# Optimization experiments

Hardware: AMD Instinct MI355X
Metric: run time of the kernel (lower is better)

Reference implementation:

```python
import jax, jax.numpy as jnp
import numpy as np

NUM_HEADS = 4
EPS = 1e-5

def _proj(x, W, b):
    # 1x1x1 Conv3d == channel-wise linear: x [B,C,H,W,D], W [Cout,Cin], b [Cout]
    return jnp.einsum('oc,bchwd->bohwd', W, x) + b[None, :, None, None, None]

def setup_inputs() -> dict:
    key = jax.random.key(0)
    ks = jax.random.split(key, 12)
    B, C, H, W, D = 2, 128, 16, 16, 16
    s = 1.0 / np.sqrt(C)
    inp = {
        'query_features': jax.random.normal(ks[0], (B, C, H, W, D), jnp.float32),
        'key_value_features': jax.random.normal(ks[1], (B, C, H, W, D), jnp.float32),
        'Wq': jax.random.normal(ks[2], (C, C), jnp.float32) * s,
        'bq': jax.random.normal(ks[3], (C,), jnp.float32) * 0.01,
        'Wk': jax.random.normal(ks[4], (C, C), jnp.float32) * s,
        'bk': jax.random.normal(ks[5], (C,), jnp.float32) * 0.01,
        'Wv': jax.random.normal(ks[6], (C, C), jnp.float32) * s,
        'bv': jax.random.normal(ks[7], (C,), jnp.float32) * 0.01,
        'Wo': jax.random.normal(ks[8], (C, C), jnp.float32) * s,
        'bo': jax.random.normal(ks[9], (C,), jnp.float32) * 0.01,
    }
    return inp

def reference(query_features, key_value_features, Wq, bq, Wk, bk, Wv, bv, Wo, bo):
    B, C, H, W, D = query_features.shape
    hd = C // NUM_HEADS  # head_dim
    N = H * W * D
    Q = _proj(query_features, Wq, bq).reshape(B, NUM_HEADS, hd, N)
    K = _proj(key_value_features, Wk, bk).reshape(B, NUM_HEADS, hd, N)
    V = _proj(key_value_features, Wv, bv).reshape(B, NUM_HEADS, hd, N)
    scale = hd ** -0.5
    attn = jnp.einsum('bhdn,bhdm->bhnm', Q, K) * scale  # [B,h,N,N]
    attn = jax.nn.softmax(attn, axis=-1)
    out = jnp.einsum('bhnm,bhdm->bhdn', attn, V).reshape(B, C, H, W, D)
    out = _proj(out, Wo, bo)
    res = query_features + out
    # InstanceNorm3d (affine=False): normalize over spatial dims per (B,C)
    mu = jnp.mean(res, axis=(2, 3, 4), keepdims=True)
    var = jnp.var(res, axis=(2, 3, 4), keepdims=True)
    return (res - mu) * jax.lax.rsqrt(var + EPS)
```

## Files before the change

### kernel.cpp

```cpp
#include <hip/hip_runtime.h>
#include <hip/hip_bf16.h>

typedef unsigned short u16;
typedef unsigned int u32;
typedef __bf16 bf16_t;
typedef bf16_t bf16x8 __attribute__((ext_vector_type(8)));
typedef float f32x4 __attribute__((ext_vector_type(4)));

#define NTOT 4096
#define CCH 128
#define QSCL 0.25503486703f

__device__ __forceinline__ float bf2f(u16 x) {
    return __uint_as_float(((u32)x) << 16);
}
__device__ __forceinline__ u32 pkbf(float a, float b) {
    __hip_bfloat162 h = __float22bfloat162_rn(make_float2(a, b));
    u32 r; __builtin_memcpy(&r, &h, 4); return r;
}
__device__ __forceinline__ u16 f2bf(float a) {
    return (u16)(pkbf(a, a) & 0xffffu);
}

__global__ __launch_bounds__(256, 4) void proj_kernel(
    const float* __restrict__ xq, const float* __restrict__ xkv,
    const float* __restrict__ Wq, const float* __restrict__ bq,
    const float* __restrict__ Wk, const float* __restrict__ bk_,
    const float* __restrict__ Wv, const float* __restrict__ bv_,
    u16* __restrict__ Qt, u16* __restrict__ Kt, u16* __restrict__ Vn)
{
    const int nt = blockIdx.x, p = blockIdx.y, b = blockIdx.z;
    const float* X    = (p == 0) ? xq : xkv;
    const float* Wf   = (p == 0) ? Wq : (p == 1) ? Wk : Wv;
    const float* bias = (p == 0) ? bq : (p == 1) ? bk_ : bv_;
    const float s = (p == 0) ? QSCL : 1.0f;
    const int n0 = nt * 64;
    const int tid = threadIdx.x;

    __shared__ u16 Xt[64 * 128];
    __shared__ u16 Wl[128 * 136];

    #pragma unroll
    for (int k = 0; k < 4; ++k) {
        int n = tid & 63;
        int c = (tid >> 6) + k * 4;
        float f[8];
        #pragma unroll
        for (int j = 0; j < 8; ++j)
            f[j] = X[((size_t)(b * CCH) + 8 * c + j) * NTOT + n0 + n];
        uint4 vv = {pkbf(f[0], f[1]), pkbf(f[2], f[3]), pkbf(f[4], f[5]), pkbf(f[6], f[7])};
        *(uint4*)(Xt + n * 128 + ((c ^ (n & 7)) * 8)) = vv;
    }
    #pragma unroll
    for (int k = 0; k < 8; ++k) {
        int id = tid + k * 256;
        int row = id >> 4;
        int off = (id & 15) * 8;
        const float* wsrc = Wf + row * 128 + off;
        float4 wa = *(const float4*)(wsrc);
        float4 wc = *(const float4*)(wsrc + 4);
        uint4 vv = {pkbf(wa.x * s, wa.y * s), pkbf(wa.z * s, wa.w * s),
                    pkbf(wc.x * s, wc.y * s), pkbf(wc.z * s, wc.w * s)};
        *(uint4*)(Wl + row * 136 + off) = vv;
    }
    __syncthreads();

    const int wave = tid >> 6, lane = tid & 63;
    const int quad = lane >> 4, l16 = lane & 15;
    f32x4 acc[8];
    #pragma unroll
    for (int cf = 0; cf < 8; ++cf) acc[cf] = (f32x4){0.f, 0.f, 0.f, 0.f};

    #pragma unroll
    for (int kk = 0; kk < 4; ++kk) {
        bf16x8 bx = *(const bf16x8*)(Xt + (wave * 16 + l16) * 128 +
                                     (((kk * 4 + quad) ^ (l16 & 7)) * 8));
        #pragma unroll
        for (int cf = 0; cf < 8; ++cf) {
            bf16x8 aw = *(const bf16x8*)(Wl + (cf * 16 + l16) * 136 + kk * 32 + quad * 8);
            acc[cf] = __builtin_amdgcn_mfma_f32_16x16x32_bf16(aw, bx, acc[cf], 0, 0, 0);
        }
    }

    const int n = n0 + wave * 16 + l16;
    #pragma unroll
    for (int cf = 0; cf < 8; ++cf) {
        float4 b4 = *(const float4*)(bias + cf * 16 + quad * 4);
        float v0 = acc[cf][0] + b4.x * s;
        float v1 = acc[cf][1] + b4.y * s;
        float v2 = acc[cf][2] + b4.z * s;
        float v3 = acc[cf][3] + b4.w * s;
        if (p < 2) {
            const int h = cf >> 1;
            const int d0 = (cf & 1) * 16 + quad * 4;
            u16* dst = (p == 0 ? Qt : Kt) + ((size_t)(b * 4 + h) * NTOT + n) * 32 + d0;
            uint2 vv = {pkbf(v0, v1), pkbf(v2, v3)};
            *(uint2*)dst = vv;
        } else {
            int c = cf * 16 + quad * 4;
            u16* dst = Vn + (size_t)(b * CCH + c) * NTOT + n;
            dst[0 * NTOT] = f2bf(v0); dst[1 * NTOT] = f2bf(v1);
            dst[2 * NTOT] = f2bf(v2); dst[3 * NTOT] = f2bf(v3);
        }
    }
}

__global__ __launch_bounds__(512, 4) void flash_attn_kernel(
    const u16* __restrict__ Qt, const u16* __restrict__ Kt,
    const u16* __restrict__ Vn, u16* __restrict__ pO, float* __restrict__ pL)
{
    const int bh = blockIdx.z, kc = blockIdx.y;
    const int wave = threadIdx.x >> 6, lane = threadIdx.x & 63;
    const int q = lane >> 4, l16 = lane & 15;
    const int q0w = blockIdx.x * 256 + wave * 32;

    const u16* Qbh = Qt + (size_t)bh * NTOT * 32;
    const u16* Kbh = Kt + (size_t)bh * NTOT * 32;
    const u16* Vg  = Vn + ((size_t)((bh >> 2) * CCH + (bh & 3) * 32)) * NTOT;

    __shared__ u16 Ksh[8 * 2048];
    __shared__ u16 Vsh[8 * 2048];

    const int kbase = kc * 1024;

    bf16x8 bq[2];
    #pragma unroll
    for (int g = 0; g < 2; ++g)
        bq[g] = *(const bf16x8*)(Qbh + (size_t)(q0w + g * 16 + l16) * 32 + q * 8);

    bf16x8 aone;
    {
        u32 oo = 0x3F803F80u;
        uint4 uo = {oo, oo, oo, oo};
        __builtin_memcpy(&aone, &uo, 16);
    }

    const int w4 = wave & 3;
    const size_t kst0 = (size_t)(kbase + w4 * 16 + l16) * 32 + q * 8;
    const size_t vst0 = (size_t)((w4 & 1) * 16 + l16) * NTOT + kbase +
                        (w4 >> 1) * 32 + q * 8;
    const int kds = w4 * 512 + lane * 8;
    const int vds = w4 * 512 + (q & 1) * 256 + l16 * 8 + (q >> 1) * 4;
    const int frd = lane * 8;

    f32x4 o[2][2];
    f32x4 ol[2];
    #pragma unroll
    for (int g = 0; g < 2; ++g) {
        o[g][0] = (f32x4){0,0,0,0};
        o[g][1] = (f32x4){0,0,0,0};
        ol[g]   = (f32x4){0,0,0,0};
    }
    const f32x4 zero = {0,0,0,0};

    for (int half = 0; half < 2; ++half) {
        if (half)
            __syncthreads();
        if (wave < 4) {
            const size_t kst = kst0 + (size_t)(half * 512) * 32;
            #pragma unroll
            for (int m = 0; m < 8; ++m) {
                uint4 kr = *(const uint4*)(Kbh + kst + m * 2048);
                *(uint4*)(&Ksh[m * 2048 + kds]) = kr;
            }
        } else {
            const size_t vst = vst0 + half * 512;
            #pragma unroll
            for (int m = 0; m < 8; ++m) {
                uint4 vr = *(const uint4*)(Vg + vst + m * 64);
                uint2 va = {vr.x, vr.y};
                uint2 vb = {vr.z, vr.w};
                *(uint2*)(&Vsh[m * 2048 + vds])       = va;
                *(uint2*)(&Vsh[m * 2048 + vds + 128]) = vb;
            }
        }
        __syncthreads();

        for (int m = 0; m < 8; ++m) {
            const int mb = m * 2048;
            bf16x8 ak[4], av[4];
            #pragma unroll
            for (int t = 0; t < 4; ++t) {
                ak[t] = *(const bf16x8*)(&Ksh[mb + t * 512 + frd]);
                av[t] = *(const bf16x8*)(&Vsh[mb + t * 512 + frd]);
            }
            f32x4 s[2][4];
            #pragma unroll
            for (int t = 0; t < 4; ++t) {
                #pragma unroll
                for (int g = 0; g < 2; ++g)
                    s[g][t] = __builtin_amdgcn_mfma_f32_16x16x32_bf16(ak[t], bq[g], zero, 0, 0, 0);
            }
            #pragma unroll
            for (int g = 0; g < 2; ++g) {
                u32 uw[8];
                #pragma unroll
                for (int t = 0; t < 4; ++t) {
                    float e0 = __builtin_amdgcn_exp2f(s[g][t][0]);
                    float e1 = __builtin_amdgcn_exp2f(s[g][t][1]);
                    float e2 = __builtin_amdgcn_exp2f(s[g][t][2]);
                    float e3 = __builtin_amdgcn_exp2f(s[g][t][3]);
                    uw[t * 2]     = pkbf(e0, e1);
                    uw[t * 2 + 1] = pkbf(e2, e3);
                }
                uint4 u0 = {uw[0], uw[1], uw[2], uw[3]};
                uint4 u1 = {uw[4], uw[5], uw[6], uw[7]};
                bf16x8 pb0, pb1;
                __builtin_memcpy(&pb0, &u0, 16);
                __builtin_memcpy(&pb1, &u1, 16);
                o[g][0] = __builtin_amdgcn_mfma_f32_16x16x32_bf16(av[0], pb0, o[g][0], 0, 0, 0);
                o[g][1] = __builtin_amdgcn_mfma_f32_16x16x32_bf16(av[1], pb0, o[g][1], 0, 0, 0);
                o[g][0] = __builtin_amdgcn_mfma_f32_16x16x32_bf16(av[2], pb1, o[g][0], 0, 0, 0);
                o[g][1] = __builtin_amdgcn_mfma_f32_16x16x32_bf16(av[3], pb1, o[g][1], 0, 0, 0);
                ol[g]   = __builtin_amdgcn_mfma_f32_16x16x32_bf16(aone,  pb0, ol[g],   0, 0, 0);
                ol[g]   = __builtin_amdgcn_mfma_f32_16x16x32_bf16(aone,  pb1, ol[g],   0, 0, 0);
            }
        }
    }

    #pragma unroll
    for (int g = 0; g < 2; ++g) {
        const size_t ob = ((size_t)(kc * 8 + bh) * NTOT + q0w + g * 16 + l16) * 32 + q * 4;
        uint2 w0 = {pkbf(o[g][0][0], o[g][0][1]), pkbf(o[g][0][2], o[g][0][3])};
        uint2 w1 = {pkbf(o[g][1][0], o[g][1][1]), pkbf(o[g][1][2], o[g][1][3])};
        *(uint2*)(pO + ob)      = w0;
        *(uint2*)(pO + ob + 16) = w1;
        if (q == 0)
            pL[(size_t)(kc * 8 + bh) * NTOT + q0w + g * 16 + l16] = ol[g][0];
    }
}

__global__ __launch_bounds__(256, 4) void outproj_kernel(
    const float* __restrict__ xq,
    const u16* __restrict__ pO, const float* __restrict__ pL,
    const float* __restrict__ Wo, const float* __restrict__ bo,
    float* __restrict__ res, float* __restrict__ partS, float* __restrict__ partQ)
{
    const int nt = blockIdx.x, ct = blockIdx.y, b = blockIdx.z;
    const int n0 = nt * 32;
    const int tid = threadIdx.x;

    __shared__ u16 Xt[32 * 128];
    __shared__ u16 Wl[64 * 136];

    #pragma unroll
    for (int k = 0; k < 2; ++k) {
        int cid = tid + k * 256;
        int n = cid >> 4;
        int ch = cid & 15;
        int bh = b * 4 + (ch >> 2);
        int d0 = (ch & 3) * 8;
        float l = 0.f;
        float v[8];
        #pragma unroll
        for (int j = 0; j < 8; ++j) v[j] = 0.f;
        #pragma unroll
        for (int kcc = 0; kcc < 4; ++kcc) {
            const size_t nrow = (size_t)(kcc * 8 + bh) * NTOT + n0 + n;
            l += pL[nrow];
            uint4 u = *(const uint4*)(pO + nrow * 32 + d0);
            const u32 uu[4] = {u.x, u.y, u.z, u.w};
            #pragma unroll
            for (int j = 0; j < 4; ++j) {
                v[2 * j]     += bf2f((u16)(uu[j] & 0xffffu));
                v[2 * j + 1] += bf2f((u16)(uu[j] >> 16));
            }
        }
        const float inv = 1.0f / l;
        uint4 vv = {pkbf(v[0] * inv, v[1] * inv), pkbf(v[2] * inv, v[3] * inv),
                    pkbf(v[4] * inv, v[5] * inv), pkbf(v[6] * inv, v[7] * inv)};
        *(uint4*)(Xt + n * 128 + ((ch ^ (n & 7)) * 8)) = vv;
    }
    #pragma unroll
    for (int k = 0; k < 4; ++k) {
        int id = tid + k * 256;
        int row = id >> 4;
        int off = (id & 15) * 8;
        const float* wsrc = Wo + (size_t)(ct * 64 + row) * 128 + off;
        float4 wa = *(const float4*)(wsrc);
        float4 wc = *(const float4*)(wsrc + 4);
        uint4 vv = {pkbf(wa.x, wa.y), pkbf(wa.z, wa.w),
                    pkbf(wc.x, wc.y), pkbf(wc.z, wc.w)};
        *(uint4*)(Wl + row * 136 + off) = vv;
    }
    __syncthreads();

    const int wave = tid >> 6, lane = tid & 63;
    const int quad = lane >> 4, l16 = lane & 15;
    const int nh = wave & 1, chh = wave >> 1;
    f32x4 acc[2];
    #pragma unroll
    for (int cf = 0; cf < 2; ++cf) acc[cf] = (f32x4){0.f, 0.f, 0.f, 0.f};

    #pragma unroll
    for (int kk = 0; kk < 4; ++kk) {
        bf16x8 bx = *(const bf16x8*)(Xt + (nh * 16 + l16) * 128 +
                                     (((kk * 4 + quad) ^ (l16 & 7)) * 8));
        #pragma unroll
        for (int cf = 0; cf < 2; ++cf) {
            bf16x8 aw = *(const bf16x8*)(Wl + (chh * 32 + cf * 16 + l16) * 136 +
                                         kk * 32 + quad * 8);
            acc[cf] = __builtin_amdgcn_mfma_f32_16x16x32_bf16(aw, bx, acc[cf], 0, 0, 0);
        }
    }

    const int n = n0 + nh * 16 + l16;
    const int tile = nt * 2 + nh;
    #pragma unroll
    for (int cf = 0; cf < 2; ++cf) {
        const int cbase = ct * 64 + chh * 32 + cf * 16 + quad * 4;
        float4 b4 = *(const float4*)(bo + cbase);
        const float bb[4] = {b4.x, b4.y, b4.z, b4.w};
        float sv[4], qv[4];
        #pragma unroll
        for (int r = 0; r < 4; ++r) {
            int c = cbase + r;
            float v = acc[cf][r] + bb[r] + xq[(size_t)(b * CCH + c) * NTOT + n];
            res[(size_t)(b * CCH + c) * NTOT + n] = v;
            sv[r] = v;
            qv[r] = v * v;
        }
        #pragma unroll
        for (int off = 1; off < 16; off <<= 1) {
            #pragma unroll
            for (int r = 0; r < 4; ++r) {
                sv[r] += __shfl_xor(sv[r], off);
                qv[r] += __shfl_xor(qv[r], off);
            }
        }
        if (l16 == 0) {
            #pragma unroll
            for (int r = 0; r < 4; ++r) {
                int c = cbase + r;
                partS[(size_t)(b * CCH + c) * 256 + tile] = sv[r];
                partQ[(size_t)(b * CCH + c) * 256 + tile] = qv[r];
            }
        }
    }
}

__global__ __launch_bounds__(256) void norm_kernel(
    const float* __restrict__ res, const float* __restrict__ partS,
    const float* __restrict__ partQ, float* __restrict__ out)
{
    const int c = blockIdx.x, b = blockIdx.y, zq = blockIdx.z;
    const int tid = threadIdx.x;
    const size_t row = (size_t)(b * CCH + c);
    __shared__ float rs[4], rq[4];
    float s = partS[row * 256 + tid];
    float q = partQ[row * 256 + tid];
    #pragma unroll
    for (int off = 1; off < 64; off <<= 1) {
        s += __shfl_xor(s, off);
        q += __shfl_xor(q, off);
    }
    const int wv = tid >> 6, ln = tid & 63;
    if (ln == 0) { rs[wv] = s; rq[wv] = q; }
    __syncthreads();
    float ts = rs[0] + rs[1] + rs[2] + rs[3];
    float tq = rq[0] + rq[1] + rq[2] + rq[3];
    float mu  = ts * (1.0f / 4096.0f);
    float var = tq * (1.0f / 4096.0f) - mu * mu;
    float inv = rsqrtf(var + 1e-5f);
    const size_t base = row * NTOT;
    const int n = tid * 4 + zq * 1024;
    float4 v = *(const float4*)(res + base + n);
    float4 o;
    o.x = (v.x - mu) * inv; o.y = (v.y - mu) * inv;
    o.z = (v.z - mu) * inv; o.w = (v.w - mu) * inv;
    *(float4*)(out + base + n) = o;
}

extern "C" void kernel_launch(void* const* d_in, const int* in_sizes, int n_in,
                              void* d_out, int out_size, void* d_ws, size_t ws_size,
                              hipStream_t stream)
{
    const float* xq  = (const float*)d_in[0];
    const float* xkv = (const float*)d_in[1];
    const float* Wq  = (const float*)d_in[2];
    const float* bq  = (const float*)d_in[3];
    const float* Wk  = (const float*)d_in[4];
    const float* bk  = (const float*)d_in[5];
    const float* Wv  = (const float*)d_in[6];
    const float* bv  = (const float*)d_in[7];
    const float* Wo  = (const float*)d_in[8];
    const float* bo  = (const float*)d_in[9];
    float* out = (float*)d_out;

    char* ws = (char*)d_ws;
    const size_t MB = (size_t)1 << 20;
    u16* Qt = (u16*)(ws + 0 * MB);
    u16* Kt = (u16*)(ws + 2 * MB);
    u16* Vn = (u16*)(ws + 4 * MB);
    u16* pO = (u16*)(ws + 6 * MB);
    float* pL = (float*)(ws + 14 * MB);
    float* res   = (float*)(ws + 16 * MB);
    float* partS = (float*)(ws + 20 * MB);
    float* partQ = (float*)(ws + 20 * MB + 262144);

    proj_kernel<<<dim3(64, 3, 2), 256, 0, stream>>>(xq, xkv, Wq, bq, Wk, bk, Wv, bv, Qt, Kt, Vn);
    flash_attn_kernel<<<dim3(16, 4, 8), 512, 0, stream>>>(Qt, Kt, Vn, pO, pL);
    outproj_kernel<<<dim3(128, 2, 2), 256, 0, stream>>>(xq, pO, pL, Wo, bo, res, partS, partQ);
    norm_kernel<<<dim3(128, 2, 4), 256, 0, stream>>>(res, partS, partQ, out);
}
```

Baseline: 121.5 us.

## Fuse instance norm into outproj via grid-wide atomic barrier

New measurement: 197.9 us. 1.63x slower.

```diff
diff --git a/kernel.cpp b/kernel.cpp
--- a/kernel.cpp
+++ b/kernel.cpp
@@ -27,15 +27,18 @@
     const float* __restrict__ Wq, const float* __restrict__ bq,
     const float* __restrict__ Wk, const float* __restrict__ bk_,
     const float* __restrict__ Wv, const float* __restrict__ bv_,
-    u16* __restrict__ Qt, u16* __restrict__ Kt, u16* __restrict__ Vn)
+    u16* __restrict__ Qt, u16* __restrict__ Kt, u16* __restrict__ Vn,
+    u32* __restrict__ cnt)
 {
     const int nt = blockIdx.x, p = blockIdx.y, b = blockIdx.z;
+    const int tid = threadIdx.x;
+    if (nt == 0 && p == 0 && b == 0 && tid < 160) cnt[tid] = 0;
+
     const float* X    = (p == 0) ? xq : xkv;
     const float* Wf   = (p == 0) ? Wq : (p == 1) ? Wk : Wv;
     const float* bias = (p == 0) ? bq : (p == 1) ? bk_ : bv_;
     const float s = (p == 0) ? QSCL : 1.0f;
     const int n0 = nt * 64;
-    const int tid = threadIdx.x;
 
     __shared__ u16 Xt[64 * 128];
     __shared__ u16 Wl[128 * 136];
@@ -234,7 +237,8 @@
     const float* __restrict__ xq,
     const u16* __restrict__ pO, const float* __restrict__ pL,
     const float* __restrict__ Wo, const float* __restrict__ bo,
-    float* __restrict__ res, float* __restrict__ partS, float* __restrict__ partQ)
+    float* __restrict__ partS, float* __restrict__ partQ,
+    float* __restrict__ out, u32* __restrict__ cnt)
 {
     const int nt = blockIdx.x, ct = blockIdx.y, b = blockIdx.z;
     const int n0 = nt * 32;
@@ -242,6 +246,7 @@
 
     __shared__ u16 Xt[32 * 128];
     __shared__ u16 Wl[64 * 136];
+    __shared__ float2 muv[64];
 
     #pragma unroll
     for (int k = 0; k < 2; ++k) {
@@ -306,6 +311,7 @@
 
     const int n = n0 + nh * 16 + l16;
     const int tile = nt * 2 + nh;
+    float vkeep[2][4];
     #pragma unroll
     for (int cf = 0; cf < 2; ++cf) {
         const int cbase = ct * 64 + chh * 32 + cf * 16 + quad * 4;
@@ -316,7 +322,7 @@
         for (int r = 0; r < 4; ++r) {
             int c = cbase + r;
             float v = acc[cf][r] + bb[r] + xq[(size_t)(b * CCH + c) * NTOT + n];
-            res[(size_t)(b * CCH + c) * NTOT + n] = v;
+            vkeep[cf][r] = v;
             sv[r] = v;
             qv[r] = v * v;
         }
@@ -337,38 +343,55 @@
             }
         }
     }
-}
-
-__global__ __launch_bounds__(256) void norm_kernel(
-    const float* __restrict__ res, const float* __restrict__ partS,
-    const float* __restrict__ partQ, float* __restrict__ out)
-{
-    const int c = blockIdx.x, b = blockIdx.y, zq = blockIdx.z;
-    const int tid = threadIdx.x;
-    const size_t row = (size_t)(b * CCH + c);
-    __shared__ float rs[4], rq[4];
-    float s = partS[row * 256 + tid];
-    float q = partQ[row * 256 + tid];
-    #pragma unroll
-    for (int off = 1; off < 64; off <<= 1) {
-        s += __shfl_xor(s, off);
-        q += __shfl_xor(q, off);
-    }
-    const int wv = tid >> 6, ln = tid & 63;
-    if (ln == 0) { rs[wv] = s; rq[wv] = q; }
+
+    __threadfence();
     __syncthreads();
-    float ts = rs[0] + rs[1] + rs[2] + rs[3];
-    float tq = rq[0] + rq[1] + rq[2] + rq[3];
-    float mu  = ts * (1.0f / 4096.0f);
-    float var = tq * (1.0f / 4096.0f) - mu * mu;
-    float inv = rsqrtf(var + 1e-5f);
-    const size_t base = row * NTOT;
-    const int n = tid * 4 + zq * 1024;
-    float4 v = *(const float4*)(res + base + n);
-    float4 o;
-    o.x = (v.x - mu) * inv; o.y = (v.y - mu) * inv;
-    o.z = (v.z - mu) * inv; o.w = (v.w - mu) * inv;
-    *(float4*)(out + base + n) = o;
+    if (tid == 0) {
+        u32 old = __hip_atomic_fetch_add(&cnt[(blockIdx.x & 7) * 16], 1u,
+                                         __ATOMIC_ACQ_REL, __HIP_MEMORY_SCOPE_AGENT);
+        if (old == 63u)
+            __hip_atomic_fetch_add(&cnt[144], 1u,
+                                   __ATOMIC_ACQ_REL, __HIP_MEMORY_SCOPE_AGENT);
+        for (int i = 0; i < (1 << 20); ++i) {
+            if (__hip_atomic_load(&cnt[144], __ATOMIC_ACQUIRE,
+                                  __HIP_MEMORY_SCOPE_AGENT) >= 8u)
+                break;
+            __builtin_amdgcn_s_sleep(16);
+        }
+    }
+    __syncthreads();
+
+    {
+        const int r = tid >> 2, part = tid & 3;
+        const size_t prow = ((size_t)(b * CCH + ct * 64 + r)) * 256 + part * 64;
+        float S = 0.f, Q = 0.f;
+        #pragma unroll
+        for (int j = 0; j < 16; ++j) {
+            float4 s4 = *(const float4*)(partS + prow + j * 4);
+            float4 q4 = *(const float4*)(partQ + prow + j * 4);
+            S += (s4.x + s4.y) + (s4.z + s4.w);
+            Q += (q4.x + q4.y) + (q4.z + q4.w);
+        }
+        S += __shfl_xor(S, 1); S += __shfl_xor(S, 2);
+        Q += __shfl_xor(Q, 1); Q += __shfl_xor(Q, 2);
+        if (part == 0) {
+            float mu  = S * (1.0f / 4096.0f);
+            float var = Q * (1.0f / 4096.0f) - mu * mu;
+            muv[r] = make_float2(mu, rsqrtf(var + 1e-5f));
+        }
+    }
+    __syncthreads();
+
+    #pragma unroll
+    for (int cf = 0; cf < 2; ++cf) {
+        const int lrb = chh * 32 + cf * 16 + quad * 4;
+        #pragma unroll
+        for (int r = 0; r < 4; ++r) {
+            float2 m = muv[lrb + r];
+            int c = ct * 64 + lrb + r;
+            out[(size_t)(b * CCH + c) * NTOT + n] = (vkeep[cf][r] - m.x) * m.y;
+        }
+    }
 }
 
 extern "C" void kernel_launch(void* const* d_in, const int* in_sizes, int n_in,
@@ -394,12 +417,11 @@
     u16* Vn = (u16*)(ws + 4 * MB);
     u16* pO = (u16*)(ws + 6 * MB);
     float* pL = (float*)(ws + 14 * MB);
-    float* res   = (float*)(ws + 16 * MB);
     float* partS = (float*)(ws + 20 * MB);
     float* partQ = (float*)(ws + 20 * MB + 262144);
-
-    proj_kernel<<<dim3(64, 3, 2), 256, 0, stream>>>(xq, xkv, Wq, bq, Wk, bk, Wv, bv, Qt, Kt, Vn);
+    u32* cnt = (u32*)(ws + 21 * MB);
+
+    proj_kernel<<<dim3(64, 3, 2), 256, 0, stream>>>(xq, xkv, Wq, bq, Wk, bk, Wv, bv, Qt, Kt, Vn, cnt);
     flash_attn_kernel<<<dim3(16, 4, 8), 512, 0, stream>>>(Qt, Kt, Vn, pO, pL);
-    outproj_kernel<<<dim3(128, 2, 2), 256, 0, stream>>>(xq, pO, pL, Wo, bo, res, partS, partQ);
-    norm_kernel<<<dim3(128, 2, 4), 256, 0, stream>>>(res, partS, partQ, out);
-}
+    outproj_kernel<<<dim3(128, 2, 2), 256, 0, stream>>>(xq, pO, pL, Wo, bo, partS, partQ, out, cnt);
+}
```
